# Kernel tuning notes

Measured on AMD Instinct MI355X. Metric: run time of the kernel, lower is better.

## Reference

```python
import jax, jax.numpy as jnp
import numpy as np

DEG = np.pi / 180.0
H_FOV = (-180.0 * DEG, 180.0 * DEG)   # azimuth fov (rad)
V_FOV = (-3.0 * DEG, 25.0 * DEG)      # elevation fov (rad), phi = -asin(z/r)
W = 2048  # int((h_fov[1]-h_fov[0]) / h_res), h_res = 360/2048 deg
H = 64    # int((v_fov[1]-v_fov[0]) / v_res), v_res = 28/64 deg
B = 8
N = 2_000_000


def setup_inputs() -> dict:
    key = jax.random.key(0)
    k1, k2, k3 = jax.random.split(key, 3)
    # realistic lidar-scale coordinates: wide xy spread, shallow z
    xyz = jax.random.normal(k1, (N, 3), jnp.float32) * jnp.array([30.0, 30.0, 3.0], jnp.float32)
    inten = jax.random.uniform(k2, (N, 1), dtype=jnp.float32)
    bs = jax.random.randint(k3, (N, 1), 0, B).astype(jnp.float32)  # batch idx stored as float col 0
    points = jnp.concatenate([bs, xyz, inten], axis=1)  # [N, 5]
    return {"points": points, "batch_size": B}


def reference(points, batch_size):
    # points: [N, 1+4] = (batch_idx, x, y, z, intensity)
    bs_idx = points[:, 0].astype(jnp.int32)
    xyz = points[:, 1:4]
    extra = points[:, 4:]

    # spherical projection: r, theta (azimuth, cw from +x), phi (elevation, cw from xy-plane)
    r = jnp.linalg.norm(xyz, axis=1, keepdims=True)                      # [N,1]
    theta = -jnp.arctan2(xyz[:, 1], xyz[:, 0])[:, None]                  # [N,1]
    phi = -jnp.arcsin(xyz[:, 2:3] / jnp.maximum(r, 1e-5))                # [N,1]

    u_n = (theta - H_FOV[0]) / (H_FOV[1] - H_FOV[0])                     # [N,1] normed col
    v_n = (phi - V_FOV[0]) / (V_FOV[1] - V_FOV[0])                       # [N,1] normed row

    mask = (u_n[:, 0] >= 0) & (u_n[:, 0] < 1) & (v_n[:, 0] >= 0) & (v_n[:, 0] < 1)

    u = (u_n[:, 0] * W).astype(jnp.int32)
    v = (v_n[:, 0] * H).astype(jnp.int32)
    # route masked-out points to an out-of-bounds index; scatter mode='drop' discards them
    u = jnp.where(mask, u, W)
    v = jnp.where(mask, v, H)

    # use_xyz=True: features = [xyz, rThetaPhi, raw_features] -> channels = 7
    features = jnp.concatenate([xyz, r, theta, phi, extra], axis=1)      # [N,7]

    rv = jnp.zeros((batch_size, H, W, features.shape[1]), points.dtype)
    rv = rv.at[bs_idx, v, u].set(features, mode='drop')
    return jnp.transpose(rv, (0, 3, 1, 2))  # [B, 7, H, W]
```

## Files before the change

kernel.cpp:

```cpp
#include <hip/hip_runtime.h>
#include <math.h>

#define W_IMG 2048
#define H_IMG 64
#define B_IMG 8
#define C_IMG 7
#define HW_IMG (H_IMG * W_IMG)
#define NPIX (B_IMG * HW_IMG)

typedef float v4f __attribute__((ext_vector_type(4)));

__device__ __forceinline__ float F(unsigned u) { return __uint_as_float(u); }
#define FMAF(a,b,c) __builtin_fmaf((a),(b),(c))

__device__ __forceinline__ float glibc_atanf(float x) {
    const float atanhi[4] = {F(0x3eed6338u), F(0x3f490fdau), F(0x3f7b985eu), F(0x3fc90fdau)};
    const float atanlo[4] = {F(0x31ac3769u), F(0x33222168u), F(0x33140fb4u), F(0x33a22168u)};
    const float aT0 = F(0x3eaaaaabu), aT1 = F(0xbe4ccccdu), aT2 = F(0x3e124925u),
                aT3 = F(0xbde38e38u), aT4 = F(0x3dba2e6eu), aT5 = F(0xbd9d8795u),
                aT6 = F(0x3d886b35u), aT7 = F(0xbd6ef16bu), aT8 = F(0x3d4bda59u),
                aT9 = F(0xbd15a221u), aT10 = F(0x3c8569d7u);

    unsigned hx = __float_as_uint(x);
    unsigned ix = hx & 0x7fffffffu;
    if (ix >= 0x4c800000u) {
        if (ix > 0x7f800000u) return x + x;
        float v = __fadd_rn(atanhi[3], atanlo[3]);
        return (hx >> 31) ? -v : v;
    }
    int id;
    float xr = x;
    if (ix < 0x3ee00000u) {
        if (ix < 0x31000000u) return x;
        id = -1;
    } else {
        xr = fabsf(x);
        if (ix < 0x3f980000u) {
            if (ix < 0x3f300000u) {
                id = 0;
                xr = __fdiv_rn(__fsub_rn(__fmul_rn(2.0f, xr), 1.0f),
                               __fadd_rn(2.0f, xr));
            } else {
                id = 1;
                xr = __fdiv_rn(__fsub_rn(xr, 1.0f), __fadd_rn(xr, 1.0f));
            }
        } else {
            if (ix < 0x401c0000u) {
                id = 2;
                xr = __fdiv_rn(__fsub_rn(xr, 1.5f),
                               __fadd_rn(1.0f, __fmul_rn(1.5f, xr)));
            } else {
                id = 3;
                xr = __fdiv_rn(-1.0f, xr);
            }
        }
    }
    float z = __fmul_rn(xr, xr);
    float w = __fmul_rn(z, z);
    float s1 = __fmul_rn(z, __fadd_rn(aT0, __fmul_rn(w, __fadd_rn(aT2,
               __fmul_rn(w, __fadd_rn(aT4, __fmul_rn(w, __fadd_rn(aT6,
               __fmul_rn(w, __fadd_rn(aT8, __fmul_rn(w, aT10)))))))))));
    float s2 = __fmul_rn(w, __fadd_rn(aT1, __fmul_rn(w, __fadd_rn(aT3,
               __fmul_rn(w, __fadd_rn(aT5, __fmul_rn(w, __fadd_rn(aT7,
               __fmul_rn(w, aT9)))))))));
    if (id < 0) return __fsub_rn(x, __fmul_rn(x, __fadd_rn(s1, s2)));
    float zz = __fsub_rn(atanhi[id],
               __fsub_rn(__fsub_rn(__fmul_rn(xr, __fadd_rn(s1, s2)), atanlo[id]), xr));
    return (hx >> 31) ? -zz : zz;
}

__device__ __forceinline__ float glibc_atan2f(float y, float x) {
    const float pi_o_2 = F(0x3fc90fdbu);
    const float pi     = F(0x40490fdbu);
    const float pi_lo  = F(0xb3bbbd2eu);
    unsigned hx = __float_as_uint(x), hy = __float_as_uint(y);
    unsigned ix = hx & 0x7fffffffu, iy = hy & 0x7fffffffu;
    if (ix > 0x7f800000u || iy > 0x7f800000u) return x + y;
    if (hx == 0x3f800000u) return glibc_atanf(y);
    unsigned m = ((hy >> 31) & 1u) | ((hx >> 30) & 2u);
    if (iy == 0) {
        switch (m) {
            case 0: case 1: return y;
            case 2: return pi;
            default: return -pi;
        }
    }
    if (ix == 0) return (m & 1u) ? -pi_o_2 : pi_o_2;
    if (ix == 0x7f800000u) {
        if (iy == 0x7f800000u) {
            switch (m) {
                case 0: return F(0x3f490fdbu);
                case 1: return -F(0x3f490fdbu);
                case 2: return __fmul_rn(3.0f, F(0x3f490fdbu));
                default: return -__fmul_rn(3.0f, F(0x3f490fdbu));
            }
        } else {
            switch (m) {
                case 0: return 0.0f;
                case 1: return -0.0f;
                case 2: return pi;
                default: return -pi;
            }
        }
    }
    if (iy == 0x7f800000u) return (m & 1u) ? -pi_o_2 : pi_o_2;

    int k = ((int)iy - (int)ix) >> 23;
    float z;
    if (k > 26) {
        z = __fadd_rn(pi_o_2, __fmul_rn(0.5f, pi_lo));
        m &= 1u;
    } else if (k < -26 && (hx >> 31)) {
        z = 0.0f;
    } else {
        z = glibc_atanf(fabsf(__fdiv_rn(y, x)));
    }
    switch (m) {
        case 0: return z;
        case 1: return __uint_as_float(__float_as_uint(z) ^ 0x80000000u);
        case 2: return __fsub_rn(pi, __fsub_rn(z, pi_lo));
        default: return __fsub_rn(__fsub_rn(z, pi_lo), pi);
    }
}

#define H0F   ((float)(-3.14159265358979323846))
#define SPANH ((float)( 6.28318530717958647692))
#define V0F   ((float)(-3.0 * 3.14159265358979323846 / 180.0))
#define SPANV ((float)((25.0 * 3.14159265358979323846 / 180.0) - \
                       (-3.0 * 3.14159265358979323846 / 180.0)))
#define RHc   (1.0f / SPANH)
#define RVc   (1.0f / SPANV)

__device__ __forceinline__ float norm_r(float x, float y, float z) {
    return __fsqrt_rn(FMAF(z, z, FMAF(y, y, __fmul_rn(x, x))));
}

__device__ __forceinline__ float fast_atan01(float t) {
    bool red = t > 0.41421357f;
    float s  = red ? ((t - 1.0f) * __builtin_amdgcn_rcpf(t + 1.0f)) : t;
    float q  = s * s;
    float p  =          -0.0909090909f;
    p = FMAF(q, p,       0.1111111111f);
    p = FMAF(q, p,      -0.1428571429f);
    p = FMAF(q, p,       0.2f);
    p = FMAF(q, p,      -0.3333333333f);
    p = FMAF(q, p,       1.0f);
    float a = s * p;
    return red ? (0.78539816339f + a) : a;
}

#define MU 0.003f
#define MV 0.001f

__device__ __forceinline__ int resolve_pix(float bsf, float x, float y, float z) {
    float r  = norm_r(x, y, z);
    float zr = z * __builtin_amdgcn_rcpf(fmaxf(r, 1e-5f));
    if (zr > 0.05240f || zr < -0.42270f) return -1;

    float ax = fabsf(x), ay = fabsf(y);
    float mx = fmaxf(ax, ay), mn = fminf(ax, ay);
    float t  = (mx > 0.0f) ? (mn * __builtin_amdgcn_rcpf(mx)) : 0.0f;
    float a  = fast_atan01(t);
    if (ay > ax) a = 1.5707963268f - a;
    if (x < 0.0f) a = 3.1415926536f - a;
    float th = (y < 0.0f) ? a : -a;

    float az  = fabsf(zr);
    float arg = az * __builtin_amdgcn_rsqf(FMAF(-zr, zr, 1.0f));
    float pa  = fast_atan01(arg);
    float ph  = (zr >= 0.0f) ? -pa : pa;

    float uf = (th - H0F) * (RHc * (float)W_IMG);
    float vf = (ph - V0F) * (RVc * (float)H_IMG);
    float ulo = floorf(uf - MU), uhi = floorf(uf + MU);
    float vlo = floorf(vf - MV), vhi = floorf(vf + MV);

    int u, v;
    if (ulo == uhi) {
        u = (int)ulo;
    } else {
        float theta = -glibc_atan2f(y, x);
        float u_n = __fmul_rn(__fsub_rn(theta, H0F), RHc);
        if (!(u_n >= 0.0f && u_n < 1.0f)) return -1;
        u = (int)__fmul_rn(u_n, (float)W_IMG);
    }
    if (u < 0 || u >= W_IMG) return -1;

    if (vlo == vhi) {
        v = (int)vlo;
    } else {
        float zre = __fdiv_rn(z, fmaxf(r, 1e-5f));
        float s   = __fsqrt_rn(FMAF(-zre, zre, 1.0f));
        float d   = __fadd_rn(1.0f, s);
        float phi = -__fmul_rn(2.0f, glibc_atan2f(zre, d));
        float v_n = __fmul_rn(__fsub_rn(phi, V0F), RVc);
        if (!(v_n >= 0.0f && v_n < 1.0f)) return -1;
        v = (int)__fmul_rn(v_n, (float)H_IMG);
    }
    if (v < 0 || v >= H_IMG) return -1;

    return (((int)bsf) * H_IMG + v) * W_IMG + u;
}

#define SC_TPB 256

__global__ void __launch_bounds__(SC_TPB)
scatter_winner(const float* __restrict__ pts, int* __restrict__ winner, int n) {
    int t = blockIdx.x * blockDim.x + threadIdx.x;
    if (t >= n) return;
    int i = n - 1 - t;
    const float* q = pts + (size_t)i * 5;
    int pix = resolve_pix(q[0], q[1], q[2], q[3]);
    if (pix < 0) return;
    if (winner[pix] >= i) return;
    atomicMax(&winner[pix], i);
}

__device__ __forceinline__ float atan01_legacy(float t) {
    float q = t * t;
    float p =          -0.0117212f;
    p = FMAF(q, p,      0.05265332f);
    p = FMAF(q, p,     -0.11643287f);
    p = FMAF(q, p,      0.19354346f);
    p = FMAF(q, p,     -0.33262347f);
    p = FMAF(q, p,      0.99997726f);
    return t * p;
}

__device__ __forceinline__ void fast_angles(float x, float y, float zr,
                                            float* theta, float* phi) {
    float ax = fabsf(x), ay = fabsf(y);
    float mx = fmaxf(ax, ay), mn = fminf(ax, ay);
    float t = (mx > 0.0f) ? (mn / mx) : 0.0f;
    float a = atan01_legacy(t);
    if (ay > ax) a = 1.57079632679f - a;
    if (x < 0.0f) a = 3.14159265359f - a;
    *theta = (y < 0.0f) ? a : -a;

    float az  = fabsf(zr);
    float arg = az / __fsqrt_rn(FMAF(-zr, zr, 1.0f));
    float pa  = atan01_legacy(arg);
    *phi = (zr >= 0.0f) ? -pa : pa;
}

typedef float v2f __attribute__((ext_vector_type(2)));

__global__ void __launch_bounds__(256)
write_output(const float* __restrict__ pts, const int* __restrict__ winner,
             float* __restrict__ out) {
    int p = blockIdx.x * blockDim.x + threadIdx.x;
    if (p >= NPIX) return;

    int wi = winner[p];

    float xv = 0.f, yv = 0.f, zv = 0.f, iv = 0.f;
    float rv = 0.f, th = 0.f, ph = 0.f;
    if (wi >= 0) {
        const float* qp = pts + (size_t)wi * 5 + 1;
        v2f q01, q23;
        __builtin_memcpy(&q01, qp + 0, sizeof(q01));
        __builtin_memcpy(&q23, qp + 2, sizeof(q23));
        xv = q01.x; yv = q01.y; zv = q23.x; iv = q23.y;
        rv = norm_r(xv, yv, zv);
        float zr = __fdiv_rn(zv, fmaxf(rv, 1e-5f));
        fast_angles(xv, yv, zr, &th, &ph);
    }

    int b  = p >> 17;
    int hw = p & (HW_IMG - 1);
    float* o = out + (size_t)b * C_IMG * HW_IMG + hw;
    __builtin_nontemporal_store(xv, o + 0 * HW_IMG);
    __builtin_nontemporal_store(yv, o + 1 * HW_IMG);
    __builtin_nontemporal_store(zv, o + 2 * HW_IMG);
    __builtin_nontemporal_store(rv, o + 3 * HW_IMG);
    __builtin_nontemporal_store(th, o + 4 * HW_IMG);
    __builtin_nontemporal_store(ph, o + 5 * HW_IMG);
    __builtin_nontemporal_store(iv, o + 6 * HW_IMG);
}

extern "C" void kernel_launch(void* const* d_in, const int* in_sizes, int n_in,
                              void* d_out, int out_size, void* d_ws, size_t ws_size,
                              hipStream_t stream) {
    const float* pts = (const float*)d_in[0];
    int n = in_sizes[0] / 5;
    if (n <= 0) return;
    int* winner = (int*)d_ws;
    float* out = (float*)d_out;

    int blocks = (n + SC_TPB - 1) / SC_TPB;
    scatter_winner<<<blocks, SC_TPB, 0, stream>>>(pts, winner, n);

    int pblocks = (NPIX + 255) / 256;
    write_output<<<pblocks, 256, 0, stream>>>(pts, winner, out);
}
```

Before: 141.0 us.

## Privatize winner buffer per XCC to localize atomics, reduce copies in output

Each scatter thread reads its XCC id from a hardware register and does its atomic max into a private copy of the winner array, one copy per XCC, so atomics stay within one die's L2 and avoid cross-die coherence traffic. The output kernel then takes the max over the 8 copies per pixel. In exchange it reads eight times as much winner data in the output pass, and it drops the early-exit check that skipped atomics when a larger index was already present. It also relies on the workspace being large enough and initialized to -1 for all copies; a fallback path keeps the single-copy version.

After: 152.7 us. 1.08x slower.

```diff
diff --git a/kernel.cpp b/kernel.cpp
--- a/kernel.cpp
+++ b/kernel.cpp
@@ -7,8 +7,10 @@
 #define C_IMG 7
 #define HW_IMG (H_IMG * W_IMG)
 #define NPIX (B_IMG * HW_IMG)
+#define NCOPY 8
 
 typedef float v4f __attribute__((ext_vector_type(4)));
+typedef float v2f __attribute__((ext_vector_type(2)));
 
 __device__ __forceinline__ float F(unsigned u) { return __uint_as_float(u); }
 #define FMAF(a,b,c) __builtin_fmaf((a),(b),(c))
@@ -202,10 +204,30 @@
     return (((int)bsf) * H_IMG + v) * W_IMG + u;
 }
 
+__device__ __forceinline__ int xcc_id() {
+    unsigned x;
+    asm volatile("s_getreg_b32 %0, hwreg(HW_REG_XCC_ID)" : "=s"(x));
+    return (int)(x & 7u);
+}
+
 #define SC_TPB 256
 
 __global__ void __launch_bounds__(SC_TPB)
-scatter_winner(const float* __restrict__ pts, int* __restrict__ winner, int n) {
+scatter_winner8(const float* __restrict__ pts, int* __restrict__ winner, int n) {
+    int t = blockIdx.x * blockDim.x + threadIdx.x;
+    if (t >= n) return;
+    int i = n - 1 - t;
+    const float* q = pts + (size_t)i * 5;
+    int pix = resolve_pix(q[0], q[1], q[2], q[3]);
+    if (pix < 0) return;
+    int* wc = winner + (size_t)xcc_id() * NPIX + pix;
+    asm volatile("global_atomic_smax %0, %1, off\n\t"
+                 "s_waitcnt vmcnt(0)"
+                 :: "v"(wc), "v"(i) : "memory");
+}
+
+__global__ void __launch_bounds__(SC_TPB)
+scatter_winner1(const float* __restrict__ pts, int* __restrict__ winner, int n) {
     int t = blockIdx.x * blockDim.x + threadIdx.x;
     if (t >= n) return;
     int i = n - 1 - t;
@@ -243,15 +265,17 @@
     *phi = (zr >= 0.0f) ? -pa : pa;
 }
 
-typedef float v2f __attribute__((ext_vector_type(2)));
-
+template <int NC>
 __global__ void __launch_bounds__(256)
-write_output(const float* __restrict__ pts, const int* __restrict__ winner,
-             float* __restrict__ out) {
+write_output_t(const float* __restrict__ pts, const int* __restrict__ winner,
+               float* __restrict__ out) {
     int p = blockIdx.x * blockDim.x + threadIdx.x;
     if (p >= NPIX) return;
 
     int wi = winner[p];
+#pragma unroll
+    for (int c = 1; c < NC; ++c)
+        wi = max(wi, winner[(size_t)c * NPIX + p]);
 
     float xv = 0.f, yv = 0.f, zv = 0.f, iv = 0.f;
     float rv = 0.f, th = 0.f, ph = 0.f;
@@ -288,8 +312,13 @@
     float* out = (float*)d_out;
 
     int blocks = (n + SC_TPB - 1) / SC_TPB;
-    scatter_winner<<<blocks, SC_TPB, 0, stream>>>(pts, winner, n);
-
     int pblocks = (NPIX + 255) / 256;
-    write_output<<<pblocks, 256, 0, stream>>>(pts, winner, out);
-}
+
+    if (ws_size >= (size_t)NCOPY * NPIX * sizeof(int)) {
+        scatter_winner8<<<blocks, SC_TPB, 0, stream>>>(pts, winner, n);
+        write_output_t<NCOPY><<<pblocks, 256, 0, stream>>>(pts, winner, out);
+    } else {
+        scatter_winner1<<<blocks, SC_TPB, 0, stream>>>(pts, winner, n);
+        write_output_t<1><<<pblocks, 256, 0, stream>>>(pts, winner, out);
+    }
+}
```

## Split winner scatter into two ordered launches and vectorize output writes by two

Applied to the files above, without the earlier changes.

The scatter pass now runs as two launches: the upper half of the points first, then the lower half. Once the high-index winners are in place, the early-exit check (winner >= i) can skip more atomics in the second pass. The output kernel now handles two adjacent pixels per thread with an int2 winner load and v2f nontemporal stores, which halves the thread count and widens memory transactions. The cost is an extra launch and a serialization point between the halves, which lowers parallelism within each scatter launch.

Measured after the change: 142.9 us. Within noise of the previous version (+1.4%).

```diff
diff --git a/kernel.cpp b/kernel.cpp
--- a/kernel.cpp
+++ b/kernel.cpp
@@ -9,6 +9,7 @@
 #define NPIX (B_IMG * HW_IMG)
 
 typedef float v4f __attribute__((ext_vector_type(4)));
+typedef float v2f __attribute__((ext_vector_type(2)));
 
 __device__ __forceinline__ float F(unsigned u) { return __uint_as_float(u); }
 #define FMAF(a,b,c) __builtin_fmaf((a),(b),(c))
@@ -205,10 +206,11 @@
 #define SC_TPB 256
 
 __global__ void __launch_bounds__(SC_TPB)
-scatter_winner(const float* __restrict__ pts, int* __restrict__ winner, int n) {
+scatter_range(const float* __restrict__ pts, int* __restrict__ winner,
+              int lo, int cnt) {
     int t = blockIdx.x * blockDim.x + threadIdx.x;
-    if (t >= n) return;
-    int i = n - 1 - t;
+    if (t >= cnt) return;
+    int i = lo + cnt - 1 - t;
     const float* q = pts + (size_t)i * 5;
     int pix = resolve_pix(q[0], q[1], q[2], q[3]);
     if (pix < 0) return;
@@ -243,39 +245,47 @@
     *phi = (zr >= 0.0f) ? -pa : pa;
 }
 
-typedef float v2f __attribute__((ext_vector_type(2)));
-
 __global__ void __launch_bounds__(256)
 write_output(const float* __restrict__ pts, const int* __restrict__ winner,
              float* __restrict__ out) {
-    int p = blockIdx.x * blockDim.x + threadIdx.x;
-    if (p >= NPIX) return;
-
-    int wi = winner[p];
-
-    float xv = 0.f, yv = 0.f, zv = 0.f, iv = 0.f;
-    float rv = 0.f, th = 0.f, ph = 0.f;
-    if (wi >= 0) {
-        const float* qp = pts + (size_t)wi * 5 + 1;
-        v2f q01, q23;
-        __builtin_memcpy(&q01, qp + 0, sizeof(q01));
-        __builtin_memcpy(&q23, qp + 2, sizeof(q23));
-        xv = q01.x; yv = q01.y; zv = q23.x; iv = q23.y;
-        rv = norm_r(xv, yv, zv);
-        float zr = __fdiv_rn(zv, fmaxf(rv, 1e-5f));
-        fast_angles(xv, yv, zr, &th, &ph);
-    }
-
-    int b  = p >> 17;
-    int hw = p & (HW_IMG - 1);
+    int t  = blockIdx.x * blockDim.x + threadIdx.x;
+    int p0 = t * 2;
+    if (p0 >= NPIX) return;
+
+    int2 w2 = *(const int2*)(winner + p0);
+    int wis[2] = {w2.x, w2.y};
+
+    float fc[C_IMG][2];
+#pragma unroll
+    for (int c = 0; c < C_IMG; ++c) { fc[c][0] = 0.f; fc[c][1] = 0.f; }
+
+#pragma unroll
+    for (int k = 0; k < 2; ++k) {
+        int wi = wis[k];
+        if (wi >= 0) {
+            const float* qp = pts + (size_t)wi * 5 + 1;
+            v2f q01, q23;
+            __builtin_memcpy(&q01, qp + 0, sizeof(q01));
+            __builtin_memcpy(&q23, qp + 2, sizeof(q23));
+            float xv = q01.x, yv = q01.y, zv = q23.x, iv = q23.y;
+            float rv = norm_r(xv, yv, zv);
+            float zr = __fdiv_rn(zv, fmaxf(rv, 1e-5f));
+            float th, ph;
+            fast_angles(xv, yv, zr, &th, &ph);
+            fc[0][k] = xv; fc[1][k] = yv; fc[2][k] = zv;
+            fc[3][k] = rv; fc[4][k] = th; fc[5][k] = ph;
+            fc[6][k] = iv;
+        }
+    }
+
+    int b  = p0 >> 17;
+    int hw = p0 & (HW_IMG - 1);
     float* o = out + (size_t)b * C_IMG * HW_IMG + hw;
-    __builtin_nontemporal_store(xv, o + 0 * HW_IMG);
-    __builtin_nontemporal_store(yv, o + 1 * HW_IMG);
-    __builtin_nontemporal_store(zv, o + 2 * HW_IMG);
-    __builtin_nontemporal_store(rv, o + 3 * HW_IMG);
-    __builtin_nontemporal_store(th, o + 4 * HW_IMG);
-    __builtin_nontemporal_store(ph, o + 5 * HW_IMG);
-    __builtin_nontemporal_store(iv, o + 6 * HW_IMG);
+#pragma unroll
+    for (int c = 0; c < C_IMG; ++c) {
+        v2f v = {fc[c][0], fc[c][1]};
+        __builtin_nontemporal_store(v, (v2f*)(o + (size_t)c * HW_IMG));
+    }
 }
 
 extern "C" void kernel_launch(void* const* d_in, const int* in_sizes, int n_in,
@@ -287,9 +297,15 @@
     int* winner = (int*)d_ws;
     float* out = (float*)d_out;
 
-    int blocks = (n + SC_TPB - 1) / SC_TPB;
-    scatter_winner<<<blocks, SC_TPB, 0, stream>>>(pts, winner, n);
-
-    int pblocks = (NPIX + 255) / 256;
+    int s = n / 2;
+    int hiCnt = n - s, loCnt = s;
+    int hiBlocks = (hiCnt + SC_TPB - 1) / SC_TPB;
+    int loBlocks = (loCnt + SC_TPB - 1) / SC_TPB;
+    scatter_range<<<hiBlocks, SC_TPB, 0, stream>>>(pts, winner, s, hiCnt);
+    if (loCnt > 0)
+        scatter_range<<<loBlocks, SC_TPB, 0, stream>>>(pts, winner, 0, loCnt);
+
+    int pthreads = NPIX / 2;
+    int pblocks = (pthreads + 255) / 256;
     write_output<<<pblocks, 256, 0, stream>>>(pts, winner, out);
 }
```
